# Optimization experiments

Measured on AMD Instinct MI355X. Metric: run time of the kernel, lower is better.

The kernel has to match this reference:

```python
import jax, jax.numpy as jnp
import numpy as np

D_MODEL = 1024
NUM_HEADS = 16
HEAD_DIM = D_MODEL // NUM_HEADS
SCALE = HEAD_DIM ** -0.5


def setup_inputs() -> dict:
    key = jax.random.key(0)
    k1, k2, k3 = jax.random.split(key, 3)
    B, N = 2, 2048
    x = jax.random.normal(k1, (B, N, D_MODEL), dtype=jnp.float32)
    w_qkv = jax.random.normal(k2, (D_MODEL, 3 * D_MODEL), dtype=jnp.float32) * (D_MODEL ** -0.5)
    b_qkv = jnp.zeros((3 * D_MODEL,), dtype=jnp.float32)
    w_proj = jax.random.normal(k3, (D_MODEL, D_MODEL), dtype=jnp.float32) * (D_MODEL ** -0.5)
    b_proj = jnp.zeros((D_MODEL,), dtype=jnp.float32)
    return {"x": x, "w_qkv": w_qkv, "b_qkv": b_qkv, "w_proj": w_proj, "b_proj": b_proj}


def reference(x, w_qkv, b_qkv, w_proj, b_proj):
    B, N, C = x.shape
    H, Hd = NUM_HEADS, HEAD_DIM
    # fused QKV projection: [B,N,3C] -> [3,B,H,N,Hd]
    qkv = (x @ w_qkv + b_qkv).reshape(B, N, 3, H, Hd).transpose(2, 0, 3, 1, 4)
    q, k, v = qkv[0], qkv[1], qkv[2]
    # manual scaled dot-product attention (full NxN scores, as in source)
    attn = jnp.einsum('bhqd,bhkd->bhqk', q, k) * SCALE
    attn = jax.nn.softmax(attn, axis=-1)
    out = jnp.einsum('bhqk,bhkd->bhqd', attn, v)  # [B,H,N,Hd]
    out = out.transpose(0, 2, 1, 3).reshape(B, N, C)
    return out @ w_proj + b_proj
```

## Files before the change

kernel.cpp:

```cpp
#include <hip/hip_runtime.h>
#include <hip/hip_bf16.h>
#include <stdint.h>

typedef __attribute__((ext_vector_type(8))) __bf16 bf16x8;
typedef __attribute__((ext_vector_type(4))) __bf16 bf16x4;
typedef __attribute__((ext_vector_type(4))) float f32x4;

#define AS1 __attribute__((address_space(1)))
#define AS3 __attribute__((address_space(3)))

__device__ __forceinline__ void load_lds16(const void* g, void* l) {
    __builtin_amdgcn_global_load_lds((const AS1 void*)g, (AS3 void*)l, 16, 0, 0);
}

constexpr float QSCALE = 0.18033688011112042f;

__device__ __forceinline__ int sigma32(int kv) {
    return (kv < 16) ? ((kv >> 2) * 8 + (kv & 3))
                     : (((kv - 16) >> 2) * 8 + 4 + ((kv - 16) & 3));
}

__global__ void cvt_x(const float4* __restrict__ x, bf16x4* __restrict__ o, int n4) {
    int i = blockIdx.x * blockDim.x + threadIdx.x;
    if (i >= n4) return;
    float4 v = x[i];
    bf16x4 r;
    r[0] = (__bf16)v.x; r[1] = (__bf16)v.y; r[2] = (__bf16)v.z; r[3] = (__bf16)v.w;
    o[i] = r;
}

__global__ void tconv(const float* __restrict__ src, __bf16* __restrict__ dst,
                      int R, int C) {
    __shared__ float tile[32][33];
    int c0 = blockIdx.x * 32, r0 = blockIdx.y * 32;
    int tx = threadIdx.x, ty = threadIdx.y;
    #pragma unroll
    for (int i = 0; i < 32; i += 8)
        tile[ty + i][tx] = src[(size_t)(r0 + ty + i) * C + c0 + tx];
    __syncthreads();
    #pragma unroll
    for (int i = 0; i < 32; i += 8)
        dst[(size_t)(c0 + ty + i) * R + r0 + tx] = (__bf16)tile[tx][ty + i];
}

template <int MODE>
__global__ __launch_bounds__(256)
void gemm128(const __bf16* __restrict__ A, const __bf16* __restrict__ Bt,
             const float* __restrict__ bias, void* __restrict__ outp,
             int M, int Nn, int K) {
    __shared__ __bf16 As[128][32];
    __shared__ __bf16 Bs[128][32];
    const int t = threadIdx.x;
    const int w = t >> 6, l = t & 63;
    const int lrow = l & 15, lhi = l >> 4;
    const int wr = (w >> 1) * 64, wc = (w & 1) * 64;
    const int m0 = blockIdx.y * 128, n0 = blockIdx.x * 128;

    f32x4 acc[4][4] = {};

    const int sr = t >> 2, sc = (t & 3) * 8;
    const __bf16* ag = A + (size_t)(m0 + sr) * K + sc;
    const __bf16* bg = Bt + (size_t)(n0 + sr) * K + sc;

    for (int kt = 0; kt < K; kt += 32) {
        load_lds16(ag, &As[sr][sc]);
        load_lds16(ag + (size_t)64 * K, &As[64 + sr][sc]);
        load_lds16(bg, &Bs[sr][sc]);
        load_lds16(bg + (size_t)64 * K, &Bs[64 + sr][sc]);
        ag += 32; bg += 32;
        __syncthreads();
        bf16x8 af[4], bfv[4];
        #pragma unroll
        for (int i = 0; i < 4; ++i)
            af[i] = *(const bf16x8*)(&As[wr + i * 16 + lrow][lhi * 8]);
        #pragma unroll
        for (int j = 0; j < 4; ++j)
            bfv[j] = *(const bf16x8*)(&Bs[wc + j * 16 + lrow][lhi * 8]);
        #pragma unroll
        for (int i = 0; i < 4; ++i)
            #pragma unroll
            for (int j = 0; j < 4; ++j)
                acc[i][j] = __builtin_amdgcn_mfma_f32_16x16x32_bf16(
                    af[i], bfv[j], acc[i][j], 0, 0, 0);
        __syncthreads();
    }

    #pragma unroll
    for (int i = 0; i < 4; ++i)
        #pragma unroll
        for (int j = 0; j < 4; ++j)
            #pragma unroll
            for (int r = 0; r < 4; ++r) {
                int row = m0 + wr + i * 16 + lhi * 4 + r;
                int col = n0 + wc + j * 16 + lrow;
                float val = acc[i][j][r] + bias[col];
                if (MODE == 0) {
                    int which = col >> 10;
                    int h = (col >> 6) & 15;
                    int d = col & 63;
                    int b = row >> 11;
                    int n = row & 2047;
                    int bh = (b << 4) + h;
                    if (which == 2) {
                        ((__bf16*)outp)[(size_t)2 * (32 * 2048 * 64) +
                                        ((size_t)bh * 64 + d) * 2048 +
                                        (n & ~31) + sigma32(n & 31)] = (__bf16)val;
                    } else {
                        if (which == 0) val *= QSCALE;
                        ((__bf16*)outp)[(size_t)which * (32 * 2048 * 64) +
                                        ((size_t)bh * 2048 + n) * 64 + d] = (__bf16)val;
                    }
                } else {
                    ((float*)outp)[(size_t)row * Nn + col] = val;
                }
            }
}

__global__ __launch_bounds__(256)
void attn_fwd(const __bf16* __restrict__ q, const __bf16* __restrict__ k,
              const __bf16* __restrict__ vt, __bf16* __restrict__ out) {
    __shared__ __bf16 KsV[2][64][64];
    __shared__ __bf16 VsV[2][64][64];
    char* ksB = (char*)KsV;
    char* vsB = (char*)VsV;

    const int t = threadIdx.x;
    const int w = t >> 6, l = t & 63;
    const int lrow = l & 15, lhi = l >> 4;
    const int bh = blockIdx.y;
    const int q0 = blockIdx.x * 64 + w * 16;

    const __bf16* qp = q + ((size_t)bh * 2048 + q0) * 64;
    bf16x8 qf0 = *(const bf16x8*)(qp + lrow * 64 + lhi * 8);
    bf16x8 qf1 = *(const bf16x8*)(qp + lrow * 64 + 32 + lhi * 8);

    f32x4 oacc[4] = {};
    float mrun = -1e30f, lsum = 0.f;

    const __bf16* kg = k + (size_t)bh * 2048 * 64;
    const __bf16* vg = vt + (size_t)bh * 64 * 2048;

    const int sr = t >> 3;
    const int sw8 = ((t & 7) ^ (sr & 7)) * 8;

    const int rsw = (lrow & 7) << 4;

    {
        char* kd = ksB + t * 16;
        char* vd = vsB + t * 16;
        load_lds16(kg + (size_t)sr * 64 + sw8, kd);
        load_lds16(kg + (size_t)(32 + sr) * 64 + sw8, kd + 4096);
        load_lds16(vg + (size_t)sr * 2048 + sw8, vd);
        load_lds16(vg + (size_t)(32 + sr) * 2048 + sw8, vd + 4096);
    }

    int cur = 0;
    for (int kv0 = 0; kv0 < 2048; kv0 += 64) {
        __syncthreads();
        if (kv0 + 64 < 2048) {
            char* kd = ksB + (cur ^ 1) * 8192 + t * 16;
            char* vd = vsB + (cur ^ 1) * 8192 + t * 16;
            load_lds16(kg + (size_t)(kv0 + 64 + sr) * 64 + sw8, kd);
            load_lds16(kg + (size_t)(kv0 + 96 + sr) * 64 + sw8, kd + 4096);
            load_lds16(vg + (size_t)sr * 2048 + kv0 + 64 + sw8, vd);
            load_lds16(vg + (size_t)(32 + sr) * 2048 + kv0 + 64 + sw8, vd + 4096);
        }
        const char* kb = ksB + cur * 8192 + lrow * 128;
        const char* vb = vsB + cur * 8192 + lrow * 128;

        f32x4 s0 = {}, s1 = {}, s2 = {}, s3 = {};
        {
            bf16x8 kf;
            kf = *(const bf16x8*)(kb + (((0 + lhi) << 4) ^ rsw));
            s0 = __builtin_amdgcn_mfma_f32_16x16x32_bf16(kf, qf0, s0, 0, 0, 0);
            kf = *(const bf16x8*)(kb + (((4 + lhi) << 4) ^ rsw));
            s0 = __builtin_amdgcn_mfma_f32_16x16x32_bf16(kf, qf1, s0, 0, 0, 0);
            kf = *(const bf16x8*)(kb + 2048 + (((0 + lhi) << 4) ^ rsw));
            s1 = __builtin_amdgcn_mfma_f32_16x16x32_bf16(kf, qf0, s1, 0, 0, 0);
            kf = *(const bf16x8*)(kb + 2048 + (((4 + lhi) << 4) ^ rsw));
            s1 = __builtin_amdgcn_mfma_f32_16x16x32_bf16(kf, qf1, s1, 0, 0, 0);
            kf = *(const bf16x8*)(kb + 4096 + (((0 + lhi) << 4) ^ rsw));
            s2 = __builtin_amdgcn_mfma_f32_16x16x32_bf16(kf, qf0, s2, 0, 0, 0);
            kf = *(const bf16x8*)(kb + 4096 + (((4 + lhi) << 4) ^ rsw));
            s2 = __builtin_amdgcn_mfma_f32_16x16x32_bf16(kf, qf1, s2, 0, 0, 0);
            kf = *(const bf16x8*)(kb + 6144 + (((0 + lhi) << 4) ^ rsw));
            s3 = __builtin_amdgcn_mfma_f32_16x16x32_bf16(kf, qf0, s3, 0, 0, 0);
            kf = *(const bf16x8*)(kb + 6144 + (((4 + lhi) << 4) ^ rsw));
            s3 = __builtin_amdgcn_mfma_f32_16x16x32_bf16(kf, qf1, s3, 0, 0, 0);
        }

        float tm;
        {
            float t0 = fmaxf(fmaxf(s0[0], s0[1]), fmaxf(s0[2], s0[3]));
            float t1 = fmaxf(fmaxf(s1[0], s1[1]), fmaxf(s1[2], s1[3]));
            float t2 = fmaxf(fmaxf(s2[0], s2[1]), fmaxf(s2[2], s2[3]));
            float t3 = fmaxf(fmaxf(s3[0], s3[1]), fmaxf(s3[2], s3[3]));
            tm = fmaxf(fmaxf(t0, t1), fmaxf(t2, t3));
        }
        tm = fmaxf(tm, __shfl_xor(tm, 16, 64));
        tm = fmaxf(tm, __shfl_xor(tm, 32, 64));
        if (!__all(tm <= mrun + 8.0f)) {
            float mn = fmaxf(mrun, tm);
            float corr = __builtin_amdgcn_exp2f(mrun - mn);
            lsum *= corr;
            #pragma unroll
            for (int dt = 0; dt < 4; ++dt)
                #pragma unroll
                for (int r = 0; r < 4; ++r) oacc[dt][r] *= corr;
            mrun = mn;
        }
        float p[16];
        #pragma unroll
        for (int r = 0; r < 4; ++r) {
            p[r]      = __builtin_amdgcn_exp2f(s0[r] - mrun);
            p[4 + r]  = __builtin_amdgcn_exp2f(s1[r] - mrun);
            p[8 + r]  = __builtin_amdgcn_exp2f(s2[r] - mrun);
            p[12 + r] = __builtin_amdgcn_exp2f(s3[r] - mrun);
        }
        float rs = 0.f;
        #pragma unroll
        for (int j = 0; j < 16; ++j) rs += p[j];
        rs += __shfl_xor(rs, 16, 64);
        rs += __shfl_xor(rs, 32, 64);
        lsum += rs;

        bf16x8 pf0, pf1;
        #pragma unroll
        for (int j = 0; j < 4; ++j) {
            pf0[j] = (__bf16)p[j];       pf0[4 + j] = (__bf16)p[4 + j];
            pf1[j] = (__bf16)p[8 + j];   pf1[4 + j] = (__bf16)p[12 + j];
        }

        #pragma unroll
        for (int dt = 0; dt < 4; ++dt) {
            bf16x8 vf;
            vf = *(const bf16x8*)(vb + dt * 2048 + (((0 + lhi) << 4) ^ rsw));
            oacc[dt] = __builtin_amdgcn_mfma_f32_16x16x32_bf16(vf, pf0, oacc[dt], 0, 0, 0);
            vf = *(const bf16x8*)(vb + dt * 2048 + (((4 + lhi) << 4) ^ rsw));
            oacc[dt] = __builtin_amdgcn_mfma_f32_16x16x32_bf16(vf, pf1, oacc[dt], 0, 0, 0);
        }
        cur ^= 1;
    }

    float inv = __builtin_amdgcn_rcpf(lsum);
    const int b = bh >> 4, h = bh & 15;
    __bf16* orow = out + ((size_t)(b * 2048 + q0 + lrow)) * 1024 + h * 64;
    #pragma unroll
    for (int dt = 0; dt < 4; ++dt) {
        bf16x4 ov;
        #pragma unroll
        for (int r = 0; r < 4; ++r) ov[r] = (__bf16)(oacc[dt][r] * inv);
        *(bf16x4*)(orow + dt * 16 + lhi * 4) = ov;
    }
}

extern "C" void kernel_launch(void* const* d_in, const int* in_sizes, int n_in,
                              void* d_out, int out_size, void* d_ws, size_t ws_size,
                              hipStream_t stream) {
    const float* x      = (const float*)d_in[0];
    const float* w_qkv  = (const float*)d_in[1];
    const float* b_qkv  = (const float*)d_in[2];
    const float* w_proj = (const float*)d_in[3];
    const float* b_proj = (const float*)d_in[4];
    float* out = (float*)d_out;

    __bf16* ws     = (__bf16*)d_ws;
    __bf16* x_bf   = ws;
    __bf16* wqkvT  = x_bf + 4096 * 1024;
    __bf16* wprojT = wqkvT + 3072 * 1024;
    __bf16* qb     = wprojT + 1024 * 1024;
    __bf16* kb     = qb + 32 * 2048 * 64;
    __bf16* vtb    = kb + 32 * 2048 * 64;
    __bf16* attn   = vtb + 32 * 2048 * 64;

    cvt_x<<<4096, 256, 0, stream>>>((const float4*)x, (bf16x4*)x_bf, 4096 * 1024 / 4);
    tconv<<<dim3(96, 32), dim3(32, 8), 0, stream>>>(w_qkv, wqkvT, 1024, 3072);
    tconv<<<dim3(32, 32), dim3(32, 8), 0, stream>>>(w_proj, wprojT, 1024, 1024);
    gemm128<0><<<dim3(24, 32), 256, 0, stream>>>(x_bf, wqkvT, b_qkv, qb, 4096, 3072, 1024);
    attn_fwd<<<dim3(32, 32), 256, 0, stream>>>(qb, kb, vtb, attn);
    gemm128<1><<<dim3(8, 32), 256, 0, stream>>>(attn, wprojT, b_proj, out, 4096, 1024, 1024);
}
```

Measured before the change: 222.0 us.

## Process two query tiles per wave in attention to reuse K/V fragments

Each wave now handles 32 query rows (two 16-row tiles) instead of 16, so every K and V fragment read from LDS feeds two MFMAs, and the grid is halved to 16x32 blocks. The row-sum cross-lane reduction moves out of the loop to the epilogue, and s_setprio is raised around the MFMA sections. Global staging pointers are now advanced incrementally. The change aims to cut LDS traffic and K/V reloads per query, at the cost of more registers and only 512 blocks, which lowers parallelism on the device.

```diff
diff --git a/kernel.cpp b/kernel.cpp
--- a/kernel.cpp
+++ b/kernel.cpp
@@ -11,6 +11,10 @@
 
 __device__ __forceinline__ void load_lds16(const void* g, void* l) {
     __builtin_amdgcn_global_load_lds((const AS1 void*)g, (AS3 void*)l, 16, 0, 0);
+}
+
+__device__ __forceinline__ float m3(float a, float b, float c) {
+    return fmaxf(fmaxf(a, b), c);
 }
 
 constexpr float QSCALE = 0.18033688011112042f;
@@ -128,21 +132,23 @@
     const int w = t >> 6, l = t & 63;
     const int lrow = l & 15, lhi = l >> 4;
     const int bh = blockIdx.y;
-    const int q0 = blockIdx.x * 64 + w * 16;
+    const int q0 = blockIdx.x * 128 + w * 32;
 
     const __bf16* qp = q + ((size_t)bh * 2048 + q0) * 64;
-    bf16x8 qf0 = *(const bf16x8*)(qp + lrow * 64 + lhi * 8);
-    bf16x8 qf1 = *(const bf16x8*)(qp + lrow * 64 + 32 + lhi * 8);
-
-    f32x4 oacc[4] = {};
-    float mrun = -1e30f, lsum = 0.f;
+    bf16x8 qfA0 = *(const bf16x8*)(qp + lrow * 64 + lhi * 8);
+    bf16x8 qfA1 = *(const bf16x8*)(qp + lrow * 64 + 32 + lhi * 8);
+    bf16x8 qfB0 = *(const bf16x8*)(qp + (16 + lrow) * 64 + lhi * 8);
+    bf16x8 qfB1 = *(const bf16x8*)(qp + (16 + lrow) * 64 + 32 + lhi * 8);
+
+    f32x4 oA[4] = {}, oB[4] = {};
+    float mA = -1e30f, mB = -1e30f;
+    float lA = 0.f, lB = 0.f;
 
     const __bf16* kg = k + (size_t)bh * 2048 * 64;
     const __bf16* vg = vt + (size_t)bh * 64 * 2048;
 
     const int sr = t >> 3;
     const int sw8 = ((t & 7) ^ (sr & 7)) * 8;
-
     const int rsw = (lrow & 7) << 4;
 
     {
@@ -154,103 +160,131 @@
         load_lds16(vg + (size_t)(32 + sr) * 2048 + sw8, vd + 4096);
     }
 
+    const __bf16* kst  = kg + (size_t)(64 + sr) * 64 + sw8;
+    const __bf16* kst2 = kst + 32 * 64;
+    const __bf16* vst  = vg + (size_t)sr * 2048 + 64 + sw8;
+    const __bf16* vst2 = vst + 32 * 2048;
+
     int cur = 0;
     for (int kv0 = 0; kv0 < 2048; kv0 += 64) {
         __syncthreads();
         if (kv0 + 64 < 2048) {
             char* kd = ksB + (cur ^ 1) * 8192 + t * 16;
             char* vd = vsB + (cur ^ 1) * 8192 + t * 16;
-            load_lds16(kg + (size_t)(kv0 + 64 + sr) * 64 + sw8, kd);
-            load_lds16(kg + (size_t)(kv0 + 96 + sr) * 64 + sw8, kd + 4096);
-            load_lds16(vg + (size_t)sr * 2048 + kv0 + 64 + sw8, vd);
-            load_lds16(vg + (size_t)(32 + sr) * 2048 + kv0 + 64 + sw8, vd + 4096);
+            load_lds16(kst, kd);
+            load_lds16(kst2, kd + 4096);
+            load_lds16(vst, vd);
+            load_lds16(vst2, vd + 4096);
+            kst += 4096; kst2 += 4096; vst += 64; vst2 += 64;
         }
         const char* kb = ksB + cur * 8192 + lrow * 128;
         const char* vb = vsB + cur * 8192 + lrow * 128;
-
-        f32x4 s0 = {}, s1 = {}, s2 = {}, s3 = {};
+        const int o0 = (lhi << 4) ^ rsw;
+        const int o4 = ((4 + lhi) << 4) ^ rsw;
+
+        f32x4 sA0 = {}, sA1 = {}, sA2 = {}, sA3 = {};
+        f32x4 sB0 = {}, sB1 = {}, sB2 = {}, sB3 = {};
+        __builtin_amdgcn_s_setprio(1);
         {
-            bf16x8 kf;
-            kf = *(const bf16x8*)(kb + (((0 + lhi) << 4) ^ rsw));
-            s0 = __builtin_amdgcn_mfma_f32_16x16x32_bf16(kf, qf0, s0, 0, 0, 0);
-            kf = *(const bf16x8*)(kb + (((4 + lhi) << 4) ^ rsw));
-            s0 = __builtin_amdgcn_mfma_f32_16x16x32_bf16(kf, qf1, s0, 0, 0, 0);
-            kf = *(const bf16x8*)(kb + 2048 + (((0 + lhi) << 4) ^ rsw));
-            s1 = __builtin_amdgcn_mfma_f32_16x16x32_bf16(kf, qf0, s1, 0, 0, 0);
-            kf = *(const bf16x8*)(kb + 2048 + (((4 + lhi) << 4) ^ rsw));
-            s1 = __builtin_amdgcn_mfma_f32_16x16x32_bf16(kf, qf1, s1, 0, 0, 0);
-            kf = *(const bf16x8*)(kb + 4096 + (((0 + lhi) << 4) ^ rsw));
-            s2 = __builtin_amdgcn_mfma_f32_16x16x32_bf16(kf, qf0, s2, 0, 0, 0);
-            kf = *(const bf16x8*)(kb + 4096 + (((4 + lhi) << 4) ^ rsw));
-            s2 = __builtin_amdgcn_mfma_f32_16x16x32_bf16(kf, qf1, s2, 0, 0, 0);
-            kf = *(const bf16x8*)(kb + 6144 + (((0 + lhi) << 4) ^ rsw));
-            s3 = __builtin_amdgcn_mfma_f32_16x16x32_bf16(kf, qf0, s3, 0, 0, 0);
-            kf = *(const bf16x8*)(kb + 6144 + (((4 + lhi) << 4) ^ rsw));
-            s3 = __builtin_amdgcn_mfma_f32_16x16x32_bf16(kf, qf1, s3, 0, 0, 0);
-        }
-
-        float tm;
-        {
-            float t0 = fmaxf(fmaxf(s0[0], s0[1]), fmaxf(s0[2], s0[3]));
-            float t1 = fmaxf(fmaxf(s1[0], s1[1]), fmaxf(s1[2], s1[3]));
-            float t2 = fmaxf(fmaxf(s2[0], s2[1]), fmaxf(s2[2], s2[3]));
-            float t3 = fmaxf(fmaxf(s3[0], s3[1]), fmaxf(s3[2], s3[3]));
-            tm = fmaxf(fmaxf(t0, t1), fmaxf(t2, t3));
-        }
-        tm = fmaxf(tm, __shfl_xor(tm, 16, 64));
-        tm = fmaxf(tm, __shfl_xor(tm, 32, 64));
-        if (!__all(tm <= mrun + 8.0f)) {
-            float mn = fmaxf(mrun, tm);
-            float corr = __builtin_amdgcn_exp2f(mrun - mn);
-            lsum *= corr;
+            bf16x8 kf0, kf1;
+#define QK_GROUP(SA, SB, BASE)                                                 \
+            kf0 = *(const bf16x8*)(kb + (BASE) + o0);                          \
+            kf1 = *(const bf16x8*)(kb + (BASE) + o4);                          \
+            SA = __builtin_amdgcn_mfma_f32_16x16x32_bf16(kf0, qfA0, SA, 0, 0, 0); \
+            SA = __builtin_amdgcn_mfma_f32_16x16x32_bf16(kf1, qfA1, SA, 0, 0, 0); \
+            SB = __builtin_amdgcn_mfma_f32_16x16x32_bf16(kf0, qfB0, SB, 0, 0, 0); \
+            SB = __builtin_amdgcn_mfma_f32_16x16x32_bf16(kf1, qfB1, SB, 0, 0, 0);
+            QK_GROUP(sA0, sB0, 0)
+            QK_GROUP(sA1, sB1, 2048)
+            QK_GROUP(sA2, sB2, 4096)
+            QK_GROUP(sA3, sB3, 6144)
+#undef QK_GROUP
+        }
+        __builtin_amdgcn_s_setprio(0);
+
+        float u0 = m3(sA0[0], sA0[1], sA0[2]);
+        float u1 = m3(sA0[3], sA1[0], sA1[1]);
+        float u2 = m3(sA1[2], sA1[3], sA2[0]);
+        float u3 = m3(sA2[1], sA2[2], sA2[3]);
+        float u4 = m3(sA3[0], sA3[1], sA3[2]);
+        float tmA = fmaxf(m3(u0, u1, u2), m3(u3, u4, sA3[3]));
+        float v0 = m3(sB0[0], sB0[1], sB0[2]);
+        float v1 = m3(sB0[3], sB1[0], sB1[1]);
+        float v2 = m3(sB1[2], sB1[3], sB2[0]);
+        float v3 = m3(sB2[1], sB2[2], sB2[3]);
+        float v4 = m3(sB3[0], sB3[1], sB3[2]);
+        float tmB = fmaxf(m3(v0, v1, v2), m3(v3, v4, sB3[3]));
+        tmA = fmaxf(tmA, __shfl_xor(tmA, 16, 64));
+        tmA = fmaxf(tmA, __shfl_xor(tmA, 32, 64));
+        tmB = fmaxf(tmB, __shfl_xor(tmB, 16, 64));
+        tmB = fmaxf(tmB, __shfl_xor(tmB, 32, 64));
+        if (!__all(tmA <= mA + 8.0f && tmB <= mB + 8.0f)) {
+            float mnA = fmaxf(mA, tmA), mnB = fmaxf(mB, tmB);
+            float cA = __builtin_amdgcn_exp2f(mA - mnA);
+            float cB = __builtin_amdgcn_exp2f(mB - mnB);
+            lA *= cA; lB *= cB;
             #pragma unroll
             for (int dt = 0; dt < 4; ++dt)
                 #pragma unroll
-                for (int r = 0; r < 4; ++r) oacc[dt][r] *= corr;
-            mrun = mn;
-        }
-        float p[16];
+                for (int r = 0; r < 4; ++r) { oA[dt][r] *= cA; oB[dt][r] *= cB; }
+            mA = mnA; mB = mnB;
+        }
+        float pA[16], pB[16];
         #pragma unroll
         for (int r = 0; r < 4; ++r) {
-            p[r]      = __builtin_amdgcn_exp2f(s0[r] - mrun);
-            p[4 + r]  = __builtin_amdgcn_exp2f(s1[r] - mrun);
-            p[8 + r]  = __builtin_amdgcn_exp2f(s2[r] - mrun);
-            p[12 + r] = __builtin_amdgcn_exp2f(s3[r] - mrun);
-        }
-        float rs = 0.f;
-        #pragma unroll
-        for (int j = 0; j < 16; ++j) rs += p[j];
-        rs += __shfl_xor(rs, 16, 64);
-        rs += __shfl_xor(rs, 32, 64);
-        lsum += rs;
-
-        bf16x8 pf0, pf1;
-        #pragma unroll
-        for (int j = 0; j < 4; ++j) {
-            pf0[j] = (__bf16)p[j];       pf0[4 + j] = (__bf16)p[4 + j];
-            pf1[j] = (__bf16)p[8 + j];   pf1[4 + j] = (__bf16)p[12 + j];
-        }
-
+            pA[r]      = __builtin_amdgcn_exp2f(sA0[r] - mA);
+            pA[4 + r]  = __builtin_amdgcn_exp2f(sA1[r] - mA);
+            pA[8 + r]  = __builtin_amdgcn_exp2f(sA2[r] - mA);
+            pA[12 + r] = __builtin_amdgcn_exp2f(sA3[r] - mA);
+            pB[r]      = __builtin_amdgcn_exp2f(sB0[r] - mB);
+            pB[4 + r]  = __builtin_amdgcn_exp2f(sB1[r] - mB);
+            pB[8 + r]  = __builtin_amdgcn_exp2f(sB2[r] - mB);
+            pB[12 + r] = __builtin_amdgcn_exp2f(sB3[r] - mB);
+        }
+        float rsA = 0.f, rsB = 0.f;
+        #pragma unroll
+        for (int j = 0; j < 16; ++j) { rsA += pA[j]; rsB += pB[j]; }
+        lA += rsA; lB += rsB;
+
+        bf16x8 pfA0, pfA1, pfB0, pfB1;
+        #pragma unroll
+        for (int j = 0; j < 8; ++j) {
+            pfA0[j] = (__bf16)pA[j]; pfA1[j] = (__bf16)pA[8 + j];
+            pfB0[j] = (__bf16)pB[j]; pfB1[j] = (__bf16)pB[8 + j];
+        }
+
+        __builtin_amdgcn_s_setprio(1);
         #pragma unroll
         for (int dt = 0; dt < 4; ++dt) {
-            bf16x8 vf;
-            vf = *(const bf16x8*)(vb + dt * 2048 + (((0 + lhi) << 4) ^ rsw));
-            oacc[dt] = __builtin_amdgcn_mfma_f32_16x16x32_bf16(vf, pf0, oacc[dt], 0, 0, 0);
-            vf = *(const bf16x8*)(vb + dt * 2048 + (((4 + lhi) << 4) ^ rsw));
-            oacc[dt] = __builtin_amdgcn_mfma_f32_16x16x32_bf16(vf, pf1, oacc[dt], 0, 0, 0);
-        }
+            bf16x8 vf0 = *(const bf16x8*)(vb + dt * 2048 + o0);
+            bf16x8 vf1 = *(const bf16x8*)(vb + dt * 2048 + o4);
+            oA[dt] = __builtin_amdgcn_mfma_f32_16x16x32_bf16(vf0, pfA0, oA[dt], 0, 0, 0);
+            oA[dt] = __builtin_amdgcn_mfma_f32_16x16x32_bf16(vf1, pfA1, oA[dt], 0, 0, 0);
+            oB[dt] = __builtin_amdgcn_mfma_f32_16x16x32_bf16(vf0, pfB0, oB[dt], 0, 0, 0);
+            oB[dt] = __builtin_amdgcn_mfma_f32_16x16x32_bf16(vf1, pfB1, oB[dt], 0, 0, 0);
+        }
+        __builtin_amdgcn_s_setprio(0);
         cur ^= 1;
     }
 
-    float inv = __builtin_amdgcn_rcpf(lsum);
+    lA += __shfl_xor(lA, 16, 64); lA += __shfl_xor(lA, 32, 64);
+    lB += __shfl_xor(lB, 16, 64); lB += __shfl_xor(lB, 32, 64);
+    float invA = __builtin_amdgcn_rcpf(lA);
+    float invB = __builtin_amdgcn_rcpf(lB);
+
     const int b = bh >> 4, h = bh & 15;
-    __bf16* orow = out + ((size_t)(b * 2048 + q0 + lrow)) * 1024 + h * 64;
+    __bf16* orowA = out + ((size_t)(b * 2048 + q0 + lrow)) * 1024 + h * 64;
+    __bf16* orowB = out + ((size_t)(b * 2048 + q0 + 16 + lrow)) * 1024 + h * 64;
     #pragma unroll
     for (int dt = 0; dt < 4; ++dt) {
-        bf16x4 ov;
-        #pragma unroll
-        for (int r = 0; r < 4; ++r) ov[r] = (__bf16)(oacc[dt][r] * inv);
-        *(bf16x4*)(orow + dt * 16 + lhi * 4) = ov;
+        bf16x4 ovA, ovB;
+        #pragma unroll
+        for (int r = 0; r < 4; ++r) {
+            ovA[r] = (__bf16)(oA[dt][r] * invA);
+            ovB[r] = (__bf16)(oB[dt][r] * invB);
+        }
+        *(bf16x4*)(orowA + dt * 16 + lhi * 4) = ovA;
+        *(bf16x4*)(orowB + dt * 16 + lhi * 4) = ovB;
     }
 }
 
@@ -277,6 +311,6 @@
     tconv<<<dim3(96, 32), dim3(32, 8), 0, stream>>>(w_qkv, wqkvT, 1024, 3072);
     tconv<<<dim3(32, 32), dim3(32, 8), 0, stream>>>(w_proj, wprojT, 1024, 1024);
     gemm128<0><<<dim3(24, 32), 256, 0, stream>>>(x_bf, wqkvT, b_qkv, qb, 4096, 3072, 1024);
-    attn_fwd<<<dim3(32, 32), 256, 0, stream>>>(qb, kb, vtb, attn);
+    attn_fwd<<<dim3(16, 32), 256, 0, stream>>>(qb, kb, vtb, attn);
     gemm128<1><<<dim3(8, 32), 256, 0, stream>>>(attn, wprojT, b_proj, out, 4096, 1024, 1024);
 }
```

Measured after the change: 218.1 us. About the same (-1.8%).
